# Kernel optimization log

Measured on AMD Instinct MI355X. Metric: run time of the kernel, lower is better.

The kernel has to match this reference:

```python
import jax, jax.numpy as jnp
import numpy as np

N, E = 50000, 800000
IN_DIM, HEADS, C1, C2, OUT_DIM = 256, 8, 64, 32, 40
NEG_SLOPE = 0.2  # PyG GATConv leaky_relu slope


def setup_inputs() -> dict:
    key = jax.random.key(0)
    ks = jax.random.split(key, 12)
    g = lambda k, shp, fan: jax.random.normal(k, shp, jnp.float32) / np.float32(np.sqrt(fan))
    return {
        "x": jax.random.normal(ks[0], (N, IN_DIM), jnp.float32),
        "edge_index": jax.random.randint(ks[1], (2, E), 0, N, dtype=jnp.int32),
        # layer 1: GATConv(IN_DIM -> C1, heads=HEADS, concat=True)
        "W1": g(ks[2], (IN_DIM, HEADS * C1), IN_DIM),
        "att_src1": g(ks[3], (HEADS, C1), C1),
        "att_dst1": g(ks[4], (HEADS, C1), C1),
        "b1": jnp.zeros((HEADS * C1,), jnp.float32),
        # layer 2: GATConv(HEADS*C1 -> C2, heads=1, concat=False)
        "W2": g(ks[5], (HEADS * C1, C2), HEADS * C1),
        "att_src2": g(ks[6], (1, C2), C2),
        "att_dst2": g(ks[7], (1, C2), C2),
        "b2": jnp.zeros((C2,), jnp.float32),
        # final linear head
        "fcW": g(ks[8], (C2, OUT_DIM), C2),
        "fcb": jnp.zeros((OUT_DIM,), jnp.float32),
    }


def gat_conv(x, src, dst, W, att_src, att_dst, bias, heads, ch, concat):
    """PyG-style GATConv: gather -> per-edge attention -> segment softmax -> scatter."""
    n = x.shape[0]
    xl = (x @ W).reshape(n, heads, ch)                       # [N,H,C]
    a_src = jnp.einsum('nhc,hc->nh', xl, att_src)            # [N,H]
    a_dst = jnp.einsum('nhc,hc->nh', xl, att_dst)
    e = jax.nn.leaky_relu(a_src[src] + a_dst[dst], NEG_SLOPE)  # [E,H]
    emax = jax.ops.segment_max(e, dst, num_segments=n)
    emax = jnp.where(jnp.isfinite(emax), emax, 0.0)
    p = jnp.exp(e - emax[dst])
    denom = jax.ops.segment_sum(p, dst, num_segments=n)
    alpha = p / (denom[dst] + 1e-16)                         # [E,H]
    out = jax.ops.segment_sum(xl[src] * alpha[:, :, None], dst, num_segments=n)  # [N,H,C]
    out = out.reshape(n, heads * ch) if concat else out.mean(axis=1)
    return out + bias


def reference(x, edge_index, W1, att_src1, att_dst1, b1,
              W2, att_src2, att_dst2, b2, fcW, fcb):
    n = x.shape[0]
    loop = jnp.arange(n, dtype=edge_index.dtype)             # add_self_loops (PyG default)
    src = jnp.concatenate([edge_index[0], loop])
    dst = jnp.concatenate([edge_index[1], loop])
    h = jax.nn.relu(gat_conv(x, src, dst, W1, att_src1, att_dst1, b1, HEADS, C1, True))
    h = jax.nn.relu(gat_conv(h, src, dst, W2, att_src2, att_dst2, b2, 1, C2, False))
    embedding = h                                            # [N, C2]
    logits = h @ fcW + fcb                                   # [N, OUT_DIM]
    return (embedding, logits)
```

## Files before the change

kernel.cpp:

```cpp
#include <hip/hip_runtime.h>
#include <hip/hip_bf16.h>
#include <math.h>

#define NEG_SLOPE 0.2f
#define PCAP 131072

typedef __attribute__((ext_vector_type(8))) short bf16x8;
typedef __attribute__((ext_vector_type(4))) float f32x4;

__device__ __forceinline__ float lrelu(float x) { return x > 0.f ? x : NEG_SLOPE * x; }
__device__ __forceinline__ float blo(unsigned u) { return __uint_as_float(u << 16); }
__device__ __forceinline__ float bhi(unsigned u) { return __uint_as_float(u & 0xffff0000u); }
__device__ __forceinline__ unsigned short f2b(float f) {
    __hip_bfloat16 b = __float2bfloat16(f);
    return *(unsigned short*)&b;
}
__device__ __forceinline__ int ktrue(int k) {
    int pl = k & 63;
    return (k & ~63) + ((pl & 3) << 4) + (pl >> 2);
}


__global__ __launch_bounds__(256) void prep_kernel(
    const float* __restrict__ W1, unsigned short* __restrict__ W1T,
    const float* __restrict__ W2, unsigned short* __restrict__ W2T,
    const int* __restrict__ ei, int E, int EL, int* __restrict__ deg,
    int* __restrict__ pfill, int* __restrict__ ofill,
    uint2* __restrict__ pedges, uint2* __restrict__ oedges,
    int PN, int b_cw)
{
    const int b = blockIdx.x;
    if (b < b_cw) {
        int i = b * 256 + threadIdx.x;
        if (i < 512 * 256) {
            int nn = i >> 8, k = i & 255;
            W1T[nn * 256 + k] = f2b(W1[k * 512 + nn]);
        } else if (i < 512 * 256 + 32 * 512) {
            int j = i - 512 * 256;
            int c = j >> 9, k = j & 511;
            W2T[c * 512 + k] = f2b(W2[ktrue(k) * 32 + c]);
        }
        return;
    }
    __shared__ int lcnt[8];
    __shared__ int lbase[8];
    const int tid = threadIdx.x;
    const int base = (b - b_cw) * 1024 + tid;
    const int e0 = base, e1 = base + 256, e2 = base + 512, e3 = base + 768;
    const bool v0 = e0 < EL, v1 = e1 < EL, v2 = e2 < EL, v3 = e3 < EL;
    int s0 = 0, s1 = 0, s2 = 0, s3 = 0;
    int d0 = 0, d1 = 0, d2 = 0, d3 = 0;
    if (v0) { if (e0 < E) { s0 = ei[e0]; d0 = ei[E + e0]; } else s0 = d0 = e0 - E; }
    if (v1) { if (e1 < E) { s1 = ei[e1]; d1 = ei[E + e1]; } else s1 = d1 = e1 - E; }
    if (v2) { if (e2 < E) { s2 = ei[e2]; d2 = ei[E + e2]; } else s2 = d2 = e2 - E; }
    if (v3) { if (e3 < E) { s3 = ei[e3]; d3 = ei[E + e3]; } else s3 = d3 = e3 - E; }
    if (v0) atomicAdd(&deg[d0 << 4], 1);
    if (v1) atomicAdd(&deg[d1 << 4], 1);
    if (v2) atomicAdd(&deg[d2 << 4], 1);
    if (v3) atomicAdd(&deg[d3 << 4], 1);
    if (tid < 8) lcnt[tid] = 0;
    __syncthreads();
    int q0 = 0, q1 = 0, q2 = 0, q3 = 0;
    int r0 = 0, r1 = 0, r2 = 0, r3 = 0;
    if (v0) { q0 = d0 / PN; r0 = atomicAdd(&lcnt[q0], 1); }
    if (v1) { q1 = d1 / PN; r1 = atomicAdd(&lcnt[q1], 1); }
    if (v2) { q2 = d2 / PN; r2 = atomicAdd(&lcnt[q2], 1); }
    if (v3) { q3 = d3 / PN; r3 = atomicAdd(&lcnt[q3], 1); }
    __syncthreads();
    if (tid < 8) lbase[tid] = atomicAdd(&pfill[tid << 4], lcnt[tid]);
    __syncthreads();
    if (v0) { int sl = lbase[q0] + r0;
        if (sl < PCAP) pedges[(size_t)q0 * PCAP + sl] = make_uint2((unsigned)s0, (unsigned)d0);
        else { int os = atomicAdd(&ofill[0], 1); oedges[os] = make_uint2((unsigned)s0, (unsigned)d0); } }
    if (v1) { int sl = lbase[q1] + r1;
        if (sl < PCAP) pedges[(size_t)q1 * PCAP + sl] = make_uint2((unsigned)s1, (unsigned)d1);
        else { int os = atomicAdd(&ofill[0], 1); oedges[os] = make_uint2((unsigned)s1, (unsigned)d1); } }
    if (v2) { int sl = lbase[q2] + r2;
        if (sl < PCAP) pedges[(size_t)q2 * PCAP + sl] = make_uint2((unsigned)s2, (unsigned)d2);
        else { int os = atomicAdd(&ofill[0], 1); oedges[os] = make_uint2((unsigned)s2, (unsigned)d2); } }
    if (v3) { int sl = lbase[q3] + r3;
        if (sl < PCAP) pedges[(size_t)q3 * PCAP + sl] = make_uint2((unsigned)s3, (unsigned)d3);
        else { int os = atomicAdd(&ofill[0], 1); oedges[os] = make_uint2((unsigned)s3, (unsigned)d3); } }
}

__global__ __launch_bounds__(256) void scan1_kernel(
    const int* __restrict__ deg, int* __restrict__ bsum, int n)
{
    __shared__ int red[256];
    int t = threadIdx.x, i = blockIdx.x * 256 + t;
    red[t] = (i < n) ? deg[i << 4] : 0;
    __syncthreads();
    for (int off = 128; off > 0; off >>= 1) {
        if (t < off) red[t] += red[t + off];
        __syncthreads();
    }
    if (t == 0) bsum[blockIdx.x] = red[0];
}

__global__ __launch_bounds__(256) void scan2_kernel(
    const int* __restrict__ bsum, int* __restrict__ bsoff, int B)
{
    __shared__ int part[256];
    int t = threadIdx.x;
    int v = (t < B) ? bsum[t] : 0;
    part[t] = v;
    __syncthreads();
    for (int off = 1; off < 256; off <<= 1) {
        int tmp = (t >= off) ? part[t - off] : 0;
        __syncthreads();
        part[t] += tmp;
        __syncthreads();
    }
    if (t < B) bsoff[t] = part[t] - v;
}

__global__ __launch_bounds__(256) void scan3_kernel(
    const int* __restrict__ deg, const int* __restrict__ bsoff,
    int* __restrict__ rowptr, int* __restrict__ cursor, int n, int EL)
{
    __shared__ int part[256];
    int t = threadIdx.x, b = blockIdx.x, i = b * 256 + t;
    int v = (i < n) ? deg[i << 4] : 0;
    part[t] = v;
    __syncthreads();
    for (int off = 1; off < 256; off <<= 1) {
        int tmp = (t >= off) ? part[t - off] : 0;
        __syncthreads();
        part[t] += tmp;
        __syncthreads();
    }
    if (i < n) {
        int r = bsoff[b] + part[t] - v;
        rowptr[i] = r;
        cursor[i << 4] = r;
    }
    if (i == n - 1) rowptr[n] = EL;
}

__global__ __launch_bounds__(256) void scatter_gemm1_kernel(
    const uint2* __restrict__ pedges, const uint2* __restrict__ oedges,
    const int* __restrict__ pfill, const int* __restrict__ ofill,
    int* __restrict__ cursor, int* __restrict__ csr_src,
    const float* __restrict__ x, const unsigned short* __restrict__ W1T,
    unsigned char* __restrict__ xl1q, float* __restrict__ ascale,
    const float* __restrict__ att_src, const float* __restrict__ att_dst,
    float* __restrict__ a_dst,
    int M, int b_sc)
{
    if (blockIdx.x < b_sc) {
        const int tid = threadIdx.x;
        const int p   = blockIdx.x & 7;
        const int bi  = blockIdx.x >> 3;
        const int str = (b_sc >> 3) * 256;
        int cnt = pfill[p << 4]; if (cnt > PCAP) cnt = PCAP;
        const uint2* pe = pedges + (size_t)p * PCAP;
        for (int i0 = bi * 256 + tid; i0 < cnt; i0 += 4 * str) {
            const int i1 = i0 + str, i2 = i0 + 2 * str, i3 = i0 + 3 * str;
            const bool w1 = i1 < cnt, w2 = i2 < cnt, w3 = i3 < cnt;
            uint2 ed0 = pe[i0];
            uint2 ed1 = w1 ? pe[i1] : ed0;
            uint2 ed2 = w2 ? pe[i2] : ed0;
            uint2 ed3 = w3 ? pe[i3] : ed0;
            int p0 = atomicAdd(&cursor[ed0.y << 4], 1);
            int p1 = w1 ? atomicAdd(&cursor[ed1.y << 4], 1) : 0;
            int p2 = w2 ? atomicAdd(&cursor[ed2.y << 4], 1) : 0;
            int p3 = w3 ? atomicAdd(&cursor[ed3.y << 4], 1) : 0;
            csr_src[p0] = ed0.x;
            if (w1) csr_src[p1] = ed1.x;
            if (w2) csr_src[p2] = ed2.x;
            if (w3) csr_src[p3] = ed3.x;
        }
        if (p == 0) {
            int oc = ofill[0];
            for (int i = bi * 256 + tid; i < oc; i += str) {
                uint2 ed = oedges[i];
                int pos = atomicAdd(&cursor[ed.y << 4], 1);
                csr_src[pos] = ed.x;
            }
        }
        return;
    }
    __shared__ unsigned short As[128 * 40];
    __shared__ unsigned short Bs[128 * 40];
    const int tt  = blockIdx.x - b_sc;
    const int nt4 = gridDim.x - b_sc;
    int tr, tc;
    if (tt < (nt4 & ~31)) { tr = ((tt >> 5) << 3) + (tt & 7); tc = (tt >> 3) & 3; }
    else                  { tr = tt >> 2;                      tc = tt & 3; }
    const int row0 = tr * 128;
    const int col0 = tc * 128;
    const int tid  = threadIdx.x;
    const int wave = tid >> 6;
    const int wrow = wave >> 1;
    const int wcol = wave & 1;
    const int lane = tid & 63;
    const int quad = lane >> 4;
    const int l15  = lane & 15;
    const int sm = tid >> 1;
    const int sk = (tid & 1) * 16;

    f32x4 acc[4][4] = {};

    for (int kb = 0; kb < 256; kb += 32) {
        uint4 a0 = make_uint4(0, 0, 0, 0), a1 = make_uint4(0, 0, 0, 0);
        if (row0 + sm < M) {
            const float4* ap = (const float4*)(x + (size_t)(row0 + sm) * 256 + kb + sk);
            float4 f0 = ap[0], f1 = ap[1], f2 = ap[2], f3 = ap[3];
            a0.x = (unsigned)f2b(f0.x) | ((unsigned)f2b(f0.y) << 16);
            a0.y = (unsigned)f2b(f0.z) | ((unsigned)f2b(f0.w) << 16);
            a0.z = (unsigned)f2b(f1.x) | ((unsigned)f2b(f1.y) << 16);
            a0.w = (unsigned)f2b(f1.z) | ((unsigned)f2b(f1.w) << 16);
            a1.x = (unsigned)f2b(f2.x) | ((unsigned)f2b(f2.y) << 16);
            a1.y = (unsigned)f2b(f2.z) | ((unsigned)f2b(f2.w) << 16);
            a1.z = (unsigned)f2b(f3.x) | ((unsigned)f2b(f3.y) << 16);
            a1.w = (unsigned)f2b(f3.z) | ((unsigned)f2b(f3.w) << 16);
        }
        uint4* adp = (uint4*)&As[sm * 40 + sk];
        adp[0] = a0; adp[1] = a1;
        const uint4* bp = (const uint4*)(W1T + (size_t)(col0 + sm) * 256 + kb + sk);
        uint4* bd = (uint4*)&Bs[sm * 40 + sk];
        bd[0] = bp[0]; bd[1] = bp[1];
        __syncthreads();
        bf16x8 af[4], bf[4];
        #pragma unroll
        for (int mf = 0; mf < 4; ++mf)
            af[mf] = *(const bf16x8*)&As[(wrow * 64 + mf * 16 + l15) * 40 + quad * 8];
        #pragma unroll
        for (int nf = 0; nf < 4; ++nf)
            bf[nf] = *(const bf16x8*)&Bs[(wcol * 64 + nf * 16 + l15) * 40 + quad * 8];
        #pragma unroll
        for (int mf = 0; mf < 4; ++mf)
            #pragma unroll
            for (int nf = 0; nf < 4; ++nf)
                acc[mf][nf] = __builtin_amdgcn_mfma_f32_16x16x32_bf16(
                    af[mf], bf[nf], acc[mf][nf], 0, 0, 0);
        __syncthreads();
    }

    const int h = tc * 2 + wcol;
    float asv[4], adv[4];
    #pragma unroll
    for (int nf = 0; nf < 4; ++nf) {
        asv[nf] = att_src[h * 64 + nf * 16 + l15];
        adv[nf] = att_dst[h * 64 + nf * 16 + l15];
    }
    #pragma unroll
    for (int mf = 0; mf < 4; ++mf) {
        #pragma unroll
        for (int r = 0; r < 4; ++r) {
            const int row = row0 + wrow * 64 + mf * 16 + quad * 4 + r;
            float v0 = acc[mf][0][r], v1 = acc[mf][1][r];
            float v2 = acc[mf][2][r], v3 = acc[mf][3][r];
            float sv = v0 * asv[0] + v1 * asv[1] + v2 * asv[2] + v3 * asv[3];
            float tv = v0 * adv[0] + v1 * adv[1] + v2 * adv[2] + v3 * adv[3];
            sv += __shfl_xor(sv, 1); tv += __shfl_xor(tv, 1);
            sv += __shfl_xor(sv, 2); tv += __shfl_xor(tv, 2);
            sv += __shfl_xor(sv, 4); tv += __shfl_xor(tv, 4);
            sv += __shfl_xor(sv, 8); tv += __shfl_xor(tv, 8);
            float m4 = fmaxf(fmaxf(fabsf(v0), fabsf(v1)), fmaxf(fabsf(v2), fabsf(v3)));
            m4 = fmaxf(m4, __shfl_xor(m4, 1));
            m4 = fmaxf(m4, __shfl_xor(m4, 2));
            m4 = fmaxf(m4, __shfl_xor(m4, 4));
            m4 = fmaxf(m4, __shfl_xor(m4, 8));
            const float invs = (m4 > 0.f) ? 127.f / m4 : 0.f;
            int q0 = __float2int_rn(v0 * invs); q0 = max(-127, min(127, q0));
            int q1 = __float2int_rn(v1 * invs); q1 = max(-127, min(127, q1));
            int q2 = __float2int_rn(v2 * invs); q2 = max(-127, min(127, q2));
            int q3 = __float2int_rn(v3 * invs); q3 = max(-127, min(127, q3));
            unsigned pkq = (unsigned)(q0 + 128) | ((unsigned)(q1 + 128) << 8) |
                           ((unsigned)(q2 + 128) << 16) | ((unsigned)(q3 + 128) << 24);
            if (row < M) {
                *(unsigned*)(xl1q + (size_t)row * 512 + h * 64 + l15 * 4) = pkq;
                if (l15 == 0) {
                    *(float2*)(ascale + (size_t)row * 16 + h * 2) =
                        make_float2(sv, m4 * (1.f / 127.f));
                    a_dst[row * 8 + h] = tv;
                }
            }
        }
    }
}

__global__ __launch_bounds__(256) void gather1_kernel(
    const int* __restrict__ rowptr, const int* __restrict__ csr_src,
    const unsigned char* __restrict__ xl1q, const float* __restrict__ ascale,
    const float* __restrict__ a_dst, const float* __restrict__ b1,
    unsigned short* __restrict__ h1, int M)
{
    int wid  = (blockIdx.x * blockDim.x + threadIdx.x) >> 6;
    int lane = threadIdx.x & 63;
    if (wid >= M) return;
    const int start = rowptr[wid], end = rowptr[wid + 1];
    const int h0 = lane >> 3;
    const float adh = a_dst[wid * 8 + h0];
    float dsum = 0.f, csum = 0.f;
    float acc0 = 0.f, acc1 = 0.f, acc2 = 0.f, acc3 = 0.f;
    float acc4 = 0.f, acc5 = 0.f, acc6 = 0.f, acc7 = 0.f;

#define G1_LOAD(AS, V, idx) do {                                              \
        if ((idx) < end) {                                                    \
            int s_ = csr_src[idx];                                            \
            AS = *(const float2*)(ascale + (size_t)s_ * 16 + h0 * 2);         \
            V  = *(const uint2*)(xl1q + (size_t)s_ * 512 + (lane << 3));      \
        } else { AS = make_float2(-1e30f, 0.f); V = make_uint2(0u, 0u); }     \
    } while (0)

#define G1_CONS(AS, V) do {                                                   \
        float p_ = __expf(lrelu((AS).x + adh));                               \
        dsum += p_;                                                           \
        float sa_ = p_ * (AS).y;                                              \
        csum += sa_;                                                          \
        acc0 += (float)( (V).x        & 0xffu) * sa_;                         \
        acc1 += (float)(((V).x >>  8) & 0xffu) * sa_;                         \
        acc2 += (float)(((V).x >> 16) & 0xffu) * sa_;                         \
        acc3 += (float)( (V).x >> 24         ) * sa_;                         \
        acc4 += (float)( (V).y        & 0xffu) * sa_;                         \
        acc5 += (float)(((V).y >>  8) & 0xffu) * sa_;                         \
        acc6 += (float)(((V).y >> 16) & 0xffu) * sa_;                         \
        acc7 += (float)( (V).y >> 24         ) * sa_;                         \
    } while (0)

    float2 as0, as1, as2, as3;
    uint2  v0, v1, v2, v3;
    G1_LOAD(as0, v0, start);
    G1_LOAD(as1, v1, start + 1);
    G1_LOAD(as2, v2, start + 2);
    G1_LOAD(as3, v3, start + 3);
    for (int j = start; j < end; j += 4) {
        float2 na0, na1, na2, na3;
        uint2  nv0, nv1, nv2, nv3;
        G1_LOAD(na0, nv0, j + 4);
        G1_LOAD(na1, nv1, j + 5);
        G1_LOAD(na2, nv2, j + 6);
        G1_LOAD(na3, nv3, j + 7);
        G1_CONS(as0, v0);
        G1_CONS(as1, v1);
        G1_CONS(as2, v2);
        G1_CONS(as3, v3);
        as0 = na0; v0 = nv0; as1 = na1; v1 = nv1;
        as2 = na2; v2 = nv2; as3 = na3; v3 = nv3;
    }
#undef G1_LOAD
#undef G1_CONS

    const float inv = 1.f / (dsum + 1e-16f);
    const float c128 = 128.f * csum;
    const int pg = lane << 3;
    float bj[8];
    #pragma unroll
    for (int j = 0; j < 8; ++j) {
        int pl = (pg + j) & 63;
        bj[j] = b1[(pg & ~63) + ((pl & 3) << 4) + (pl >> 2)];
    }
    float o0 = fmaxf((acc0 - c128) * inv + bj[0], 0.f);
    float o1 = fmaxf((acc1 - c128) * inv + bj[1], 0.f);
    float o2 = fmaxf((acc2 - c128) * inv + bj[2], 0.f);
    float o3 = fmaxf((acc3 - c128) * inv + bj[3], 0.f);
    float o4 = fmaxf((acc4 - c128) * inv + bj[4], 0.f);
    float o5 = fmaxf((acc5 - c128) * inv + bj[5], 0.f);
    float o6 = fmaxf((acc6 - c128) * inv + bj[6], 0.f);
    float o7 = fmaxf((acc7 - c128) * inv + bj[7], 0.f);
    uint4 pk;
    pk.x = (unsigned)f2b(o0) | ((unsigned)f2b(o1) << 16);
    pk.y = (unsigned)f2b(o2) | ((unsigned)f2b(o3) << 16);
    pk.z = (unsigned)f2b(o4) | ((unsigned)f2b(o5) << 16);
    pk.w = (unsigned)f2b(o6) | ((unsigned)f2b(o7) << 16);
    ((uint4*)(h1 + (size_t)wid * 512))[lane] = pk;
}

__global__ __launch_bounds__(256) void gemm2_mfma_kernel(
    const unsigned short* __restrict__ h1, const unsigned short* __restrict__ W2T,
    const float* __restrict__ att_src2, const float* __restrict__ att_dst2,
    unsigned short* __restrict__ xl2b, float* __restrict__ a_src2, float* __restrict__ a_dst2,
    int M)
{
    __shared__ unsigned short As[128 * 72];
    __shared__ unsigned short Bs[32 * 72];
    const int tid  = threadIdx.x;
    const int row0 = blockIdx.x * 128;
    const int wv   = tid >> 6;
    const int lane = tid & 63;
    const int quad = lane >> 4;
    const int l15  = lane & 15;

    f32x4 acc[2][2] = {};

    for (int kb = 0; kb < 512; kb += 64) {
        #pragma unroll
        for (int i = 0; i < 4; ++i) {
            int u = tid + 256 * i;
            int r = u >> 3;
            int kq = (u & 7) * 8;
            uint4 v = make_uint4(0, 0, 0, 0);
            if (row0 + r < M)
                v = *(const uint4*)(h1 + (size_t)(row0 + r) * 512 + kb + kq);
            *(uint4*)&As[r * 72 + kq] = v;
        }
        {
            int r = tid >> 3;
            int kq = (tid & 7) * 8;
            *(uint4*)&Bs[r * 72 + kq] = *(const uint4*)(W2T + (size_t)r * 512 + kb + kq);
        }
        __syncthreads();

        #pragma unroll
        for (int ks = 0; ks < 2; ++ks) {
            bf16x8 af[2], bf[2];
            #pragma unroll
            for (int mf = 0; mf < 2; ++mf)
                af[mf] = *(const bf16x8*)&As[(wv * 32 + mf * 16 + l15) * 72 + ks * 32 + quad * 8];
            #pragma unroll
            for (int nf = 0; nf < 2; ++nf)
                bf[nf] = *(const bf16x8*)&Bs[(nf * 16 + l15) * 72 + ks * 32 + quad * 8];
            #pragma unroll
            for (int mf = 0; mf < 2; ++mf)
                #pragma unroll
                for (int nf = 0; nf < 2; ++nf)
                    acc[mf][nf] = __builtin_amdgcn_mfma_f32_16x16x32_bf16(
                        af[mf], bf[nf], acc[mf][nf], 0, 0, 0);
        }
        __syncthreads();
    }

    float as2v[2], ad2v[2];
    #pragma unroll
    for (int nf = 0; nf < 2; ++nf) {
        as2v[nf] = att_src2[nf * 16 + l15];
        ad2v[nf] = att_dst2[nf * 16 + l15];
    }
    #pragma unroll
    for (int mf = 0; mf < 2; ++mf) {
        #pragma unroll
        for (int r = 0; r < 4; ++r) {
            const int row = row0 + wv * 32 + mf * 16 + quad * 4 + r;
            float v0 = acc[mf][0][r], v1 = acc[mf][1][r];
            float sv = v0 * as2v[0] + v1 * as2v[1];
            float tv = v0 * ad2v[0] + v1 * ad2v[1];
            sv += __shfl_xor(sv, 1); tv += __shfl_xor(tv, 1);
            sv += __shfl_xor(sv, 2); tv += __shfl_xor(tv, 2);
            sv += __shfl_xor(sv, 4); tv += __shfl_xor(tv, 4);
            sv += __shfl_xor(sv, 8); tv += __shfl_xor(tv, 8);
            if (row < M) {
                xl2b[(size_t)row * 32 + l15]      = f2b(v0);
                xl2b[(size_t)row * 32 + 16 + l15] = f2b(v1);
                if (l15 == 0) { a_src2[row] = sv; a_dst2[row] = tv; }
            }
        }
    }
}

__global__ __launch_bounds__(256) void gather2_head_kernel(
    const int* __restrict__ rowptr, const int* __restrict__ csr_src,
    const unsigned short* __restrict__ xl2b, const float* __restrict__ a_src2,
    const float* __restrict__ a_dst2, const float* __restrict__ b2,
    const float* __restrict__ fcW, const float* __restrict__ fcb,
    float* __restrict__ emb, float* __restrict__ logits, int M)
{
    __shared__ float sw[32][40];
    for (int i = threadIdx.x; i < 32 * 40; i += 256) sw[i / 40][i % 40] = fcW[i];
    __syncthreads();
    int wid  = (blockIdx.x * blockDim.x + threadIdx.x) >> 6;
    int lane = threadIdx.x & 63;
    if (wid >= M) return;
    const int start = rowptr[wid], end = rowptr[wid + 1];
    const float ad = a_dst2[wid];
    const int g  = lane >> 4;
    const int c2 = lane & 15;

#define G2_LOAD(A, U, idx) do {                                               \
        if ((idx) < end) {                                                    \
            int s_ = csr_src[idx];                                            \
            A = a_src2[s_];                                                   \
            U = *(const unsigned*)(xl2b + (size_t)s_ * 32 + 2 * c2);          \
        } else { A = -1e30f; U = 0u; }                                        \
    } while (0)

    float dsum = 0.f;
    float accx = 0.f, accy = 0.f;
    float a0, a1;
    unsigned u0, u1;
    G2_LOAD(a0, u0, start + g);
    G2_LOAD(a1, u1, start + g + 4);
    for (int j = start + g; j < end; j += 8) {
        float na0, na1;
        unsigned nu0, nu1;
        G2_LOAD(na0, nu0, j + 8);
        G2_LOAD(na1, nu1, j + 12);
        {
            float p = __expf(lrelu(a0 + ad));
            dsum += p;
            accx += p * blo(u0);
            accy += p * bhi(u0);
        }
        {
            float p = __expf(lrelu(a1 + ad));
            dsum += p;
            accx += p * blo(u1);
            accy += p * bhi(u1);
        }
        a0 = na0; u0 = nu0; a1 = na1; u1 = nu1;
    }
#undef G2_LOAD
    dsum += __shfl_xor(dsum, 16); accx += __shfl_xor(accx, 16); accy += __shfl_xor(accy, 16);
    dsum += __shfl_xor(dsum, 32); accx += __shfl_xor(accx, 32); accy += __shfl_xor(accy, 32);
    const float inv = 1.f / (dsum + 1e-16f);
    const float2 b2v = *(const float2*)(b2 + 2 * c2);
    float ex = fmaxf(accx * inv + b2v.x, 0.f);
    float ey = fmaxf(accy * inv + b2v.y, 0.f);
    if (g == 0) *(float2*)(emb + (size_t)wid * 32 + 2 * c2) = make_float2(ex, ey);
    const int col = (lane < 40) ? lane : 0;
    float lsum = (lane < 40) ? fcb[col] : 0.f;
    #pragma unroll
    for (int k = 0; k < 16; ++k) {
        float vx = __shfl(ex, k);
        float vy = __shfl(ey, k);
        lsum += vx * sw[2 * k][col] + vy * sw[2 * k + 1][col];
    }
    if (lane < 40) logits[(size_t)wid * 40 + lane] = lsum;
}

extern "C" void kernel_launch(void* const* d_in, const int* in_sizes, int n_in,
                              void* d_out, int out_size, void* d_ws, size_t ws_size,
                              hipStream_t stream)
{
    const float* x   = (const float*)d_in[0];
    const int*   ei  = (const int*)d_in[1];
    const float* W1  = (const float*)d_in[2];
    const float* as1 = (const float*)d_in[3];
    const float* ad1 = (const float*)d_in[4];
    const float* b1  = (const float*)d_in[5];
    const float* W2  = (const float*)d_in[6];
    const float* as2 = (const float*)d_in[7];
    const float* ad2 = (const float*)d_in[8];
    const float* b2  = (const float*)d_in[9];
    const float* fcW = (const float*)d_in[10];
    const float* fcb = (const float*)d_in[11];

    const int n  = in_sizes[0] / 256;
    const int e  = in_sizes[1] / 2;
    const int el = e + n;
    const int pn = (((n + 7) / 8) + 63) & ~63;

    char* ws = (char*)d_ws;
    size_t off = 0;
    unsigned short* w1t  = (unsigned short*)(ws + off); off += (size_t)512 * 256 * 2;
    unsigned short* w2t  = (unsigned short*)(ws + off); off += (size_t)32 * 512 * 2;
    unsigned char*  xl1q = (unsigned char*)(ws + off);  off += (size_t)n * 512;
    float* ascale = (float*)(ws + off); off += (size_t)n * 16 * 4;
    unsigned short* h1   = (unsigned short*)(ws + off); off += (size_t)n * 512 * 2;
    unsigned short* xl2b = (unsigned short*)(ws + off); off += (size_t)n * 32 * 2;
    float* a_dst1 = (float*)(ws + off); off += (size_t)n * 8 * 4;
    float* a_src2 = (float*)(ws + off); off += (size_t)n * 4;
    float* a_dst2 = (float*)(ws + off); off += (size_t)n * 4;
    int*   deg    = (int*)(ws + off);   off += (size_t)n * 16 * 4;
    int*   pfill  = (int*)(ws + off);   off += 8 * 16 * 4;
    int*   ofill  = (int*)(ws + off);   off += 16 * 4;
    int*   cursor = (int*)(ws + off);   off += (size_t)n * 16 * 4;
    int*   rowptr = (int*)(ws + off);   off += (size_t)(n + 1) * 4;
    int*   csr_src= (int*)(ws + off);   off += (size_t)el * 4;
    int*   bsum   = (int*)(ws + off);   off += 256 * 4;
    int*   bsoff  = (int*)(ws + off);   off += 256 * 4;

    uint2* pedges = (uint2*)h1;
    uint2* oedges = (uint2*)h1 + (size_t)8 * PCAP;

    float* emb    = (float*)d_out;
    float* logits = (float*)d_out + (size_t)n * 32;

    hipMemsetAsync(deg, 0, ((size_t)n * 16 + 8 * 16 + 16) * 4, stream);

    const int b_cw = (512 * 256 + 32 * 512 + 255) / 256;
    const int b_dg = (el + 1023) / 1024;
    prep_kernel<<<b_cw + b_dg, 256, 0, stream>>>(
        W1, w1t, W2, w2t, ei, e, el, deg, pfill, ofill, pedges, oedges, pn, b_cw);

    const int nb = (n + 255) / 256;
    scan1_kernel<<<nb, 256, 0, stream>>>(deg, bsum, n);
    scan2_kernel<<<1, 256, 0, stream>>>(bsum, bsoff, nb);
    scan3_kernel<<<nb, 256, 0, stream>>>(deg, bsoff, rowptr, cursor, n, el);

    const int b_sc = 832;
    const int n_tiles_y = (n + 127) / 128;
    scatter_gemm1_kernel<<<b_sc + 4 * n_tiles_y, 256, 0, stream>>>(
        pedges, oedges, pfill, ofill, cursor, csr_src,
        x, w1t, xl1q, ascale, as1, ad1, a_dst1, n, b_sc);

    gather1_kernel<<<((size_t)n * 64 + 255) / 256, 256, 0, stream>>>(
        rowptr, csr_src, xl1q, ascale, a_dst1, b1, h1, n);
    gemm2_mfma_kernel<<<(n + 127) / 128, 256, 0, stream>>>(
        h1, w2t, as2, ad2, xl2b, a_src2, a_dst2, n);
    gather2_head_kernel<<<((size_t)n * 64 + 255) / 256, 256, 0, stream>>>(
        rowptr, csr_src, xl2b, a_src2, a_dst2, b2, fcW, fcb, emb, logits, n);
}
```

Baseline: 402.4 us.

## Pack bucketed edges into 32-bit words and store pre-scaled CSR byte offsets

Bucketed edges now hold the local destination in the high 16 bits and the source in the low 16 bits, halving the staging traffic between prep and scatter. The CSR array stores the source index pre-shifted by 9, a byte offset into the quantized features, so both gather kernels derive their addresses with shifts instead of multiplies. gather1's software prefetch depth grows from 4 to 6 edges, and leaky ReLU becomes fmaxf. This relies on N fitting in 16 bits and on src<<9 fitting in an int, and the deeper prefetch uses more registers.

Measured after the change: 417.4 us. 1.04x slower.

```diff
diff --git a/kernel.cpp b/kernel.cpp
--- a/kernel.cpp
+++ b/kernel.cpp
@@ -8,7 +8,7 @@
 typedef __attribute__((ext_vector_type(8))) short bf16x8;
 typedef __attribute__((ext_vector_type(4))) float f32x4;
 
-__device__ __forceinline__ float lrelu(float x) { return x > 0.f ? x : NEG_SLOPE * x; }
+__device__ __forceinline__ float lrelu(float x) { return fmaxf(x, NEG_SLOPE * x); }
 __device__ __forceinline__ float blo(unsigned u) { return __uint_as_float(u << 16); }
 __device__ __forceinline__ float bhi(unsigned u) { return __uint_as_float(u & 0xffff0000u); }
 __device__ __forceinline__ unsigned short f2b(float f) {
@@ -26,7 +26,7 @@
     const float* __restrict__ W2, unsigned short* __restrict__ W2T,
     const int* __restrict__ ei, int E, int EL, int* __restrict__ deg,
     int* __restrict__ pfill, int* __restrict__ ofill,
-    uint2* __restrict__ pedges, uint2* __restrict__ oedges,
+    unsigned* __restrict__ pedges, uint2* __restrict__ oedges,
     int PN, int b_cw)
 {
     const int b = blockIdx.x;
@@ -70,16 +70,16 @@
     if (tid < 8) lbase[tid] = atomicAdd(&pfill[tid << 4], lcnt[tid]);
     __syncthreads();
     if (v0) { int sl = lbase[q0] + r0;
-        if (sl < PCAP) pedges[(size_t)q0 * PCAP + sl] = make_uint2((unsigned)s0, (unsigned)d0);
+        if (sl < PCAP) pedges[(size_t)q0 * PCAP + sl] = ((unsigned)(d0 - q0 * PN) << 16) | (unsigned)s0;
         else { int os = atomicAdd(&ofill[0], 1); oedges[os] = make_uint2((unsigned)s0, (unsigned)d0); } }
     if (v1) { int sl = lbase[q1] + r1;
-        if (sl < PCAP) pedges[(size_t)q1 * PCAP + sl] = make_uint2((unsigned)s1, (unsigned)d1);
+        if (sl < PCAP) pedges[(size_t)q1 * PCAP + sl] = ((unsigned)(d1 - q1 * PN) << 16) | (unsigned)s1;
         else { int os = atomicAdd(&ofill[0], 1); oedges[os] = make_uint2((unsigned)s1, (unsigned)d1); } }
     if (v2) { int sl = lbase[q2] + r2;
-        if (sl < PCAP) pedges[(size_t)q2 * PCAP + sl] = make_uint2((unsigned)s2, (unsigned)d2);
+        if (sl < PCAP) pedges[(size_t)q2 * PCAP + sl] = ((unsigned)(d2 - q2 * PN) << 16) | (unsigned)s2;
         else { int os = atomicAdd(&ofill[0], 1); oedges[os] = make_uint2((unsigned)s2, (unsigned)d2); } }
     if (v3) { int sl = lbase[q3] + r3;
-        if (sl < PCAP) pedges[(size_t)q3 * PCAP + sl] = make_uint2((unsigned)s3, (unsigned)d3);
+        if (sl < PCAP) pedges[(size_t)q3 * PCAP + sl] = ((unsigned)(d3 - q3 * PN) << 16) | (unsigned)s3;
         else { int os = atomicAdd(&ofill[0], 1); oedges[os] = make_uint2((unsigned)s3, (unsigned)d3); } }
 }
 
@@ -138,44 +138,45 @@
 }
 
 __global__ __launch_bounds__(256) void scatter_gemm1_kernel(
-    const uint2* __restrict__ pedges, const uint2* __restrict__ oedges,
+    const unsigned* __restrict__ pedges, const uint2* __restrict__ oedges,
     const int* __restrict__ pfill, const int* __restrict__ ofill,
-    int* __restrict__ cursor, int* __restrict__ csr_src,
+    int* __restrict__ cursor, int* __restrict__ csr_off,
     const float* __restrict__ x, const unsigned short* __restrict__ W1T,
     unsigned char* __restrict__ xl1q, float* __restrict__ ascale,
     const float* __restrict__ att_src, const float* __restrict__ att_dst,
     float* __restrict__ a_dst,
-    int M, int b_sc)
+    int M, int PN, int b_sc)
 {
     if (blockIdx.x < b_sc) {
         const int tid = threadIdx.x;
         const int p   = blockIdx.x & 7;
         const int bi  = blockIdx.x >> 3;
         const int str = (b_sc >> 3) * 256;
+        const int pbase = p * PN;
         int cnt = pfill[p << 4]; if (cnt > PCAP) cnt = PCAP;
-        const uint2* pe = pedges + (size_t)p * PCAP;
+        const unsigned* pe = pedges + (size_t)p * PCAP;
         for (int i0 = bi * 256 + tid; i0 < cnt; i0 += 4 * str) {
             const int i1 = i0 + str, i2 = i0 + 2 * str, i3 = i0 + 3 * str;
             const bool w1 = i1 < cnt, w2 = i2 < cnt, w3 = i3 < cnt;
-            uint2 ed0 = pe[i0];
-            uint2 ed1 = w1 ? pe[i1] : ed0;
-            uint2 ed2 = w2 ? pe[i2] : ed0;
-            uint2 ed3 = w3 ? pe[i3] : ed0;
-            int p0 = atomicAdd(&cursor[ed0.y << 4], 1);
-            int p1 = w1 ? atomicAdd(&cursor[ed1.y << 4], 1) : 0;
-            int p2 = w2 ? atomicAdd(&cursor[ed2.y << 4], 1) : 0;
-            int p3 = w3 ? atomicAdd(&cursor[ed3.y << 4], 1) : 0;
-            csr_src[p0] = ed0.x;
-            if (w1) csr_src[p1] = ed1.x;
-            if (w2) csr_src[p2] = ed2.x;
-            if (w3) csr_src[p3] = ed3.x;
+            unsigned u0 = pe[i0];
+            unsigned u1 = w1 ? pe[i1] : u0;
+            unsigned u2 = w2 ? pe[i2] : u0;
+            unsigned u3 = w3 ? pe[i3] : u0;
+            int p0 = atomicAdd(&cursor[(pbase + (int)(u0 >> 16)) << 4], 1);
+            int p1 = w1 ? atomicAdd(&cursor[(pbase + (int)(u1 >> 16)) << 4], 1) : 0;
+            int p2 = w2 ? atomicAdd(&cursor[(pbase + (int)(u2 >> 16)) << 4], 1) : 0;
+            int p3 = w3 ? atomicAdd(&cursor[(pbase + (int)(u3 >> 16)) << 4], 1) : 0;
+            csr_off[p0] = (int)((u0 & 0xffffu) << 9);
+            if (w1) csr_off[p1] = (int)((u1 & 0xffffu) << 9);
+            if (w2) csr_off[p2] = (int)((u2 & 0xffffu) << 9);
+            if (w3) csr_off[p3] = (int)((u3 & 0xffffu) << 9);
         }
         if (p == 0) {
             int oc = ofill[0];
             for (int i = bi * 256 + tid; i < oc; i += str) {
                 uint2 ed = oedges[i];
                 int pos = atomicAdd(&cursor[ed.y << 4], 1);
-                csr_src[pos] = ed.x;
+                csr_off[pos] = (int)(ed.x << 9);
             }
         }
         return;
@@ -282,7 +283,7 @@
 }
 
 __global__ __launch_bounds__(256) void gather1_kernel(
-    const int* __restrict__ rowptr, const int* __restrict__ csr_src,
+    const int* __restrict__ rowptr, const int* __restrict__ csr_off,
     const unsigned char* __restrict__ xl1q, const float* __restrict__ ascale,
     const float* __restrict__ a_dst, const float* __restrict__ b1,
     unsigned short* __restrict__ h1, int M)
@@ -293,20 +294,23 @@
     const int start = rowptr[wid], end = rowptr[wid + 1];
     const int h0 = lane >> 3;
     const float adh = a_dst[wid * 8 + h0];
+    const char* asbase = (const char*)ascale + (h0 << 3);
+    const unsigned char* xbase = xl1q + (lane << 3);
     float dsum = 0.f, csum = 0.f;
     float acc0 = 0.f, acc1 = 0.f, acc2 = 0.f, acc3 = 0.f;
     float acc4 = 0.f, acc5 = 0.f, acc6 = 0.f, acc7 = 0.f;
 
 #define G1_LOAD(AS, V, idx) do {                                              \
         if ((idx) < end) {                                                    \
-            int s_ = csr_src[idx];                                            \
-            AS = *(const float2*)(ascale + (size_t)s_ * 16 + h0 * 2);         \
-            V  = *(const uint2*)(xl1q + (size_t)s_ * 512 + (lane << 3));      \
+            int o_ = csr_off[idx];                                            \
+            AS = *(const float2*)(asbase + (o_ >> 3));                        \
+            V  = *(const uint2*)(xbase + o_);                                 \
         } else { AS = make_float2(-1e30f, 0.f); V = make_uint2(0u, 0u); }     \
     } while (0)
 
 #define G1_CONS(AS, V) do {                                                   \
-        float p_ = __expf(lrelu((AS).x + adh));                               \
+        float x_ = (AS).x + adh;                                              \
+        float p_ = __expf(fmaxf(x_, NEG_SLOPE * x_));                         \
         dsum += p_;                                                           \
         float sa_ = p_ * (AS).y;                                              \
         csum += sa_;                                                          \
@@ -320,25 +324,31 @@
         acc7 += (float)( (V).y >> 24         ) * sa_;                         \
     } while (0)
 
-    float2 as0, as1, as2, as3;
-    uint2  v0, v1, v2, v3;
+    float2 as0, as1, as2, as3, as4, as5;
+    uint2  v0, v1, v2, v3, v4, v5;
     G1_LOAD(as0, v0, start);
     G1_LOAD(as1, v1, start + 1);
     G1_LOAD(as2, v2, start + 2);
     G1_LOAD(as3, v3, start + 3);
-    for (int j = start; j < end; j += 4) {
-        float2 na0, na1, na2, na3;
-        uint2  nv0, nv1, nv2, nv3;
-        G1_LOAD(na0, nv0, j + 4);
-        G1_LOAD(na1, nv1, j + 5);
-        G1_LOAD(na2, nv2, j + 6);
-        G1_LOAD(na3, nv3, j + 7);
+    G1_LOAD(as4, v4, start + 4);
+    G1_LOAD(as5, v5, start + 5);
+    for (int j = start; j < end; j += 6) {
+        float2 na0, na1, na2, na3, na4, na5;
+        uint2  nv0, nv1, nv2, nv3, nv4, nv5;
+        G1_LOAD(na0, nv0, j + 6);
+        G1_LOAD(na1, nv1, j + 7);
+        G1_LOAD(na2, nv2, j + 8);
+        G1_LOAD(na3, nv3, j + 9);
+        G1_LOAD(na4, nv4, j + 10);
+        G1_LOAD(na5, nv5, j + 11);
         G1_CONS(as0, v0);
         G1_CONS(as1, v1);
         G1_CONS(as2, v2);
         G1_CONS(as3, v3);
-        as0 = na0; v0 = nv0; as1 = na1; v1 = nv1;
-        as2 = na2; v2 = nv2; as3 = na3; v3 = nv3;
+        G1_CONS(as4, v4);
+        G1_CONS(as5, v5);
+        as0 = na0; v0 = nv0; as1 = na1; v1 = nv1; as2 = na2; v2 = nv2;
+        as3 = na3; v3 = nv3; as4 = na4; v4 = nv4; as5 = na5; v5 = nv5;
     }
 #undef G1_LOAD
 #undef G1_CONS
@@ -450,7 +460,7 @@
 }
 
 __global__ __launch_bounds__(256) void gather2_head_kernel(
-    const int* __restrict__ rowptr, const int* __restrict__ csr_src,
+    const int* __restrict__ rowptr, const int* __restrict__ csr_off,
     const unsigned short* __restrict__ xl2b, const float* __restrict__ a_src2,
     const float* __restrict__ a_dst2, const float* __restrict__ b2,
     const float* __restrict__ fcW, const float* __restrict__ fcb,
@@ -466,12 +476,13 @@
     const float ad = a_dst2[wid];
     const int g  = lane >> 4;
     const int c2 = lane & 15;
+    const char* xbase = (const char*)xl2b + (c2 << 2);
 
 #define G2_LOAD(A, U, idx) do {                                               \
         if ((idx) < end) {                                                    \
-            int s_ = csr_src[idx];                                            \
-            A = a_src2[s_];                                                   \
-            U = *(const unsigned*)(xl2b + (size_t)s_ * 32 + 2 * c2);          \
+            int o_ = csr_off[idx];                                            \
+            A = *(const float*)((const char*)a_src2 + (o_ >> 7));             \
+            U = *(const unsigned*)(xbase + (o_ >> 3));                        \
         } else { A = -1e30f; U = 0u; }                                        \
     } while (0)
 
@@ -487,13 +498,15 @@
         G2_LOAD(na0, nu0, j + 8);
         G2_LOAD(na1, nu1, j + 12);
         {
-            float p = __expf(lrelu(a0 + ad));
+            float xv = a0 + ad;
+            float p = __expf(fmaxf(xv, NEG_SLOPE * xv));
             dsum += p;
             accx += p * blo(u0);
             accy += p * bhi(u0);
         }
         {
-            float p = __expf(lrelu(a1 + ad));
+            float xv = a1 + ad;
+            float p = __expf(fmaxf(xv, NEG_SLOPE * xv));
             dsum += p;
             accx += p * blo(u1);
             accy += p * bhi(u1);
@@ -557,12 +570,12 @@
     int*   ofill  = (int*)(ws + off);   off += 16 * 4;
     int*   cursor = (int*)(ws + off);   off += (size_t)n * 16 * 4;
     int*   rowptr = (int*)(ws + off);   off += (size_t)(n + 1) * 4;
-    int*   csr_src= (int*)(ws + off);   off += (size_t)el * 4;
+    int*   csr_off= (int*)(ws + off);   off += (size_t)el * 4;
     int*   bsum   = (int*)(ws + off);   off += 256 * 4;
     int*   bsoff  = (int*)(ws + off);   off += 256 * 4;
 
-    uint2* pedges = (uint2*)h1;
-    uint2* oedges = (uint2*)h1 + (size_t)8 * PCAP;
+    unsigned* pedges = (unsigned*)h1;
+    uint2* oedges = (uint2*)((char*)h1 + (size_t)8 * PCAP * 4);
 
     float* emb    = (float*)d_out;
     float* logits = (float*)d_out + (size_t)n * 32;
@@ -582,13 +595,13 @@
     const int b_sc = 832;
     const int n_tiles_y = (n + 127) / 128;
     scatter_gemm1_kernel<<<b_sc + 4 * n_tiles_y, 256, 0, stream>>>(
-        pedges, oedges, pfill, ofill, cursor, csr_src,
-        x, w1t, xl1q, ascale, as1, ad1, a_dst1, n, b_sc);
+        pedges, oedges, pfill, ofill, cursor, csr_off,
+        x, w1t, xl1q, ascale, as1, ad1, a_dst1, n, pn, b_sc);
 
     gather1_kernel<<<((size_t)n * 64 + 255) / 256, 256, 0, stream>>>(
-        rowptr, csr_src, xl1q, ascale, a_dst1, b1, h1, n);
+        rowptr, csr_off, xl1q, ascale, a_dst1, b1, h1, n);
     gemm2_mfma_kernel<<<(n + 127) / 128, 256, 0, stream>>>(
         h1, w2t, as2, ad2, xl2b, a_src2, a_dst2, n);
     gather2_head_kernel<<<((size_t)n * 64 + 255) / 256, 256, 0, stream>>>(
-        rowptr, csr_src, xl2b, a_src2, a_dst2, b2, fcW, fcb, emb, logits, n);
-}
+        rowptr, csr_off, xl2b, a_src2, a_dst2, b2, fcW, fcb, emb, logits, n);
+}
```
